# Kernel optimization log

Measured on AMD Instinct MI355X. Metric: run time of the kernel, lower is better.

Reference implementation:

```python
import jax, jax.numpy as jnp
import numpy as np

HIDDEN = 512
N_DRUG = 2000
N_REACTION = 10000
N_EDGES = 400000


def setup_inputs() -> dict:
    key = jax.random.key(0)
    ks = jax.random.split(key, 6)
    z_drug = jax.random.normal(ks[0], (N_DRUG, HIDDEN), dtype=jnp.float32)
    z_reaction = jax.random.normal(ks[1], (N_REACTION, HIDDEN), dtype=jnp.float32)
    row = jax.random.randint(ks[2], (N_EDGES,), 0, N_DRUG, dtype=jnp.int64)
    col = jax.random.randint(ks[3], (N_EDGES,), 0, N_REACTION, dtype=jnp.int64)
    # Linear weights in torch layout: (out_features, in_features)
    W1 = jax.random.normal(ks[4], (HIDDEN, 2 * HIDDEN), dtype=jnp.float32) * (1.0 / np.sqrt(2 * HIDDEN))
    b1 = jnp.zeros((HIDDEN,), dtype=jnp.float32)
    W2 = jax.random.normal(ks[5], (1, HIDDEN), dtype=jnp.float32) * (1.0 / np.sqrt(HIDDEN))
    b2 = jnp.zeros((1,), dtype=jnp.float32)
    return {"z_drug": z_drug, "z_reaction": z_reaction, "row": row, "col": col,
            "W1": W1, "b1": b1, "W2": W2, "b2": b2}


def reference(z_drug, z_reaction, row, col, W1, b1, W2, b2):
    # gather + concat: [E, 2H]
    z = jnp.concatenate([z_drug[row], z_reaction[col]], axis=-1)
    h = jax.nn.relu(jnp.einsum('eh,oh->eo', z, W1) + b1)  # [E, H]
    out = jnp.einsum('eh,oh->eo', h, W2) + b2             # [E, 1]
    return out.reshape(-1)
```

## Files before the change

kernel.cpp:

```cpp
#include <hip/hip_runtime.h>
#include <stdint.h>

#define HIDDEN 512
#define NDRUG 2000
#define NREACT 10000
#define NEDGE 400000

#define NBKT 320
#define SLOT 2048
#define CSTRIDE 16
#define NSCAT 128
#define EPB ((NEDGE + NSCAT - 1) / NSCAT)

#define BPB2 2
#define EBLK (NBKT * BPB2)
#define MAXSL 1024
#define HRSTRIDE 520
#define ETHREADS 512

typedef __attribute__((ext_vector_type(8))) _Float16 f16x8;
typedef __attribute__((ext_vector_type(2))) _Float16 f16x2;
typedef __attribute__((ext_vector_type(4))) float f32x4;
typedef __attribute__((ext_vector_type(8))) float f32x8;
typedef __attribute__((ext_vector_type(4))) float float4v;
typedef __attribute__((ext_vector_type(4))) _Float16 f16x4;

#if defined(__has_builtin)
#if __has_builtin(__builtin_amdgcn_fdot2)
#define HAVE_FDOT2 1
#endif
#endif

__global__ __launch_bounds__(256) void w1prep(const float* __restrict__ W1,
                                              _Float16* __restrict__ WL,
                                              _Float16* __restrict__ WR,
                                              int* __restrict__ cursor) {
  const int b = blockIdx.x;
  const int tid = threadIdx.x;
  if (b < 128) {
    const int nth = 128 * 256;
    const int NQ = HIDDEN * 2 * HIDDEN / 4;
    for (int i = b * 256 + tid; i < NQ; i += nth) {
      int e = i * 4;
      int o = e >> 10, j = e & 1023;
      float4v v = *reinterpret_cast<const float4v*>(W1 + e);
      f16x4 q; q[0]=(_Float16)v[0]; q[1]=(_Float16)v[1]; q[2]=(_Float16)v[2]; q[3]=(_Float16)v[3];
      if (j < HIDDEN) *reinterpret_cast<f16x4*>(WL + o * HIDDEN + j) = q;
      else            *reinterpret_cast<f16x4*>(WR + o * HIDDEN + (j - HIDDEN)) = q;
    }
  } else {
    int i = (b - 128) * 256 + tid;
    if (i < NBKT) cursor[i * CSTRIDE] = i * SLOT;
  }
}

#define BM 64
#define BN 128
#define BK 32
#define GEMMBLKS 756

__global__ __launch_bounds__(256) void gemm_scatter(
    const float* __restrict__ z_drug, const float* __restrict__ z_react,
    const _Float16* __restrict__ BL, const _Float16* __restrict__ BR,
    const float* __restrict__ bias,
    const int* __restrict__ row, const int* __restrict__ col,
    _Float16* __restrict__ Hd, _Float16* __restrict__ Hr,
    int* __restrict__ cursor, uint64_t* __restrict__ pk)
{
  __shared__ _Float16 As[BM * BK];
  __shared__ _Float16 Bs[BN * BK];
  __shared__ int lhist[NBKT];
  __shared__ int lbase[NBKT];

  const int bid = blockIdx.x;
  const int tid = threadIdx.x;

  if (bid >= GEMMBLKS) {
    const int sb = bid - GEMMBLKS;
    const int e0 = sb * EPB;
    const int e1 = (e0 + EPB < NEDGE) ? e0 + EPB : NEDGE;
    for (int i = tid; i < NBKT; i += 256) lhist[i] = 0;
    __syncthreads();
    for (int e = e0 + tid; e < e1; e += 256)
      atomicAdd(&lhist[col[e] >> 5], 1);
    __syncthreads();
    for (int i = tid; i < NBKT; i += 256) {
      int cnt = lhist[i];
      lbase[i] = cnt ? atomicAdd(&cursor[i * CSTRIDE], cnt) : 0;
      lhist[i] = 0;
    }
    __syncthreads();
    for (int e = e0 + tid; e < e1; e += 256) {
      int c = col[e];
      int r = row[e];
      int bkt = c >> 5;
      int lo = atomicAdd(&lhist[bkt], 1);
      pk[lbase[bkt] + lo] = ((uint64_t)e << 25) | ((uint64_t)r << 14) | (uint64_t)c;
    }
    return;
  }

  const int z = (bid >= 128) ? 1 : 0;
  const int t = z ? bid - 128 : bid;
  const int mb = t >> 2;
  const int nb = t & 3;
  const int M = (z == 0) ? NDRUG : NREACT;
  const float* A = (z == 0) ? z_drug : z_react;
  const _Float16* B = (z == 0) ? BL : BR;
  _Float16* C = (z == 0) ? Hd : Hr;
  const bool has_bias = (z == 0);
  const int K = HIDDEN, N = HIDDEN;

  const int lane = tid & 63;
  const int wid = tid >> 6;
  const int wn = wid;

  f32x4 acc[4][2];
#pragma unroll
  for (int i = 0; i < 4; ++i)
#pragma unroll
    for (int j = 0; j < 2; ++j) acc[i][j] = (f32x4){0.f, 0.f, 0.f, 0.f};

  const int row0 = mb * BM;
  const int col0 = nb * BN;
  const int r0 = tid >> 2;
  const int q0 = tid & 3;
  const int srow = lane >> 2;
  const int scol = (lane & 3) * 8;

  for (int kt = 0; kt < K; kt += BK) {
    int rA = row0 + r0;
    rA = rA < M ? rA : M - 1;
    f32x8 va = *reinterpret_cast<const f32x8*>(A + (size_t)rA * K + kt + q0 * 8);
    f16x8 afh = __builtin_convertvector(va, f16x8);
    __syncthreads();
    *reinterpret_cast<f16x8*>(As + r0 * BK + q0 * 8) = afh;
#pragma unroll
    for (int i = 0; i < 2; ++i) {
      int rB = col0 + wid * 32 + i * 16 + srow;
      const _Float16* gB = B + (size_t)rB * K + kt + scol;
      _Float16* lB = Bs + (wid * 32 + i * 16) * BK;
      __builtin_amdgcn_global_load_lds(
          (const __attribute__((address_space(1))) void*)gB,
          (__attribute__((address_space(3))) void*)lB, 16, 0, 0);
    }
    __syncthreads();

    const int fr = lane & 15;
    const int kg = (lane >> 4) * 8;
    f16x8 af[4], bfr[2];
#pragma unroll
    for (int mi = 0; mi < 4; ++mi)
      af[mi] = *reinterpret_cast<const f16x8*>(As + (mi * 16 + fr) * BK + kg);
#pragma unroll
    for (int ni = 0; ni < 2; ++ni)
      bfr[ni] = *reinterpret_cast<const f16x8*>(Bs + (wn * 32 + ni * 16 + fr) * BK + kg);
#pragma unroll
    for (int mi = 0; mi < 4; ++mi)
#pragma unroll
      for (int ni = 0; ni < 2; ++ni)
        acc[mi][ni] = __builtin_amdgcn_mfma_f32_16x16x32_f16(af[mi], bfr[ni], acc[mi][ni], 0, 0, 0);
  }

  const int crow = (lane >> 4) * 4;
  const int ccol = lane & 15;
#pragma unroll
  for (int ni = 0; ni < 2; ++ni) {
    const int gc = col0 + wn * 32 + ni * 16 + ccol;
    const float bv = has_bias ? bias[gc] : 0.0f;
#pragma unroll
    for (int mi = 0; mi < 4; ++mi) {
#pragma unroll
      for (int j = 0; j < 4; ++j) {
        const int gr = row0 + mi * 16 + crow + j;
        if (gr < M) C[(size_t)gr * N + gc] = (_Float16)(acc[mi][ni][j] + bv);
      }
    }
  }
}

__global__ __launch_bounds__(ETHREADS) void edge_kernel(
    const _Float16* __restrict__ Hd, const _Float16* __restrict__ Hr,
    const uint64_t* __restrict__ pk, const int* __restrict__ cursor,
    const float* __restrict__ W2, const float* __restrict__ b2,
    float* __restrict__ out)
{
  __shared__ _Float16 hrs[32 * HRSTRIDE];
  __shared__ uint64_t raw[MAXSL];
  __shared__ uint64_t spk[MAXSL];
  __shared__ int qdesc[MAXSL / 4 + 32];
  __shared__ int cnt[32], cb[32], cnt2[32], qoff[32];
  __shared__ int nqs;

  const int bid = blockIdx.x;
  const int xcd = bid & 7;
  const int idx = bid >> 3;
  const int bucket = xcd * 40 + (idx >> 1);
  const int slice = idx & 1;
  const int base = bucket * SLOT;
  const int count = cursor[bucket * CSTRIDE] - base;
  const int per = (count + BPB2 - 1) / BPB2;
  const int s = slice * per;
  const int e_end0 = (s + per < count) ? s + per : count;
  const int n = (e_end0 > s) ? e_end0 - s : 0;

  const int tid = threadIdx.x;
  const int lane = tid & 63;
  const int li = lane & 15;
  const int wv = tid >> 6;
  const int gid = wv * 4 + (lane >> 4);

#pragma unroll
  for (int rr2 = 0; rr2 < 4; ++rr2) {
    int rr = wv * 4 + rr2;
    int gr = bucket * 32 + rr;
    gr = (gr < NREACT) ? gr : NREACT - 1;
    const _Float16* src = Hr + (size_t)gr * HIDDEN + lane * 8;
    _Float16* dst = hrs + rr * HRSTRIDE;
    __builtin_amdgcn_global_load_lds(
        (const __attribute__((address_space(1))) void*)src,
        (__attribute__((address_space(3))) void*)dst, 16, 0, 0);
  }

  f16x8 w2v[4];
#pragma unroll
  for (int k = 0; k < 4; ++k) {
    const float* p = W2 + li * 8 + k * 128;
    f16x8 q;
#pragma unroll
    for (int j = 0; j < 8; ++j) q[j] = (_Float16)p[j];
    w2v[k] = q;
  }
  const float bias2 = *b2;
  const f16x8 zero8 = (f16x8)(_Float16)0;

  if (tid < 32) { cnt[tid] = 0; cnt2[tid] = 0; }
  __syncthreads();
  for (int i = tid; i < n; i += ETHREADS) {
    uint64_t p = pk[base + s + i];
    raw[i] = p;
    atomicAdd(&cnt[(int)(p & 31)], 1);
  }
  __syncthreads();
  if (tid == 0) {
    int acc = 0, qa = 0;
    for (int j = 0; j < 32; ++j) {
      cb[j] = acc; acc += cnt[j];
      qoff[j] = qa; qa += (cnt[j] + 3) >> 2;
    }
    nqs = qa;
  }
  __syncthreads();
  for (int i = tid; i < n; i += ETHREADS) {
    uint64_t p = raw[i];
    int lc = (int)(p & 31);
    int lo = atomicAdd(&cnt2[lc], 1);
    spk[cb[lc] + lo] = p;
  }
  __syncthreads();
  if (tid < 32) {
    int j = tid, st = cb[j], len = cnt[j], o = qoff[j];
    for (int q = 0; q < len; q += 4) {
      int cn = len - q; cn = (cn < 4) ? cn : 4;
      qdesc[o++] = j | ((st + q) << 5) | (cn << 16);
    }
  }
  __syncthreads();

  const int nq = nqs;
  for (int q = gid; q < nq; q += 32) {
    const int d = qdesc[q];
    const int lc = d & 31;
    const int st = (d >> 5) & 2047;
    const int cn = (d >> 16) & 7;

    const _Float16* hd[4];
    int si[4];
#pragma unroll
    for (int j = 0; j < 4; ++j) {
      int jj = (j < cn) ? j : cn - 1;
      uint64_t p = spk[st + jj];
      si[j] = (int)(p >> 25);
      hd[j] = Hd + (size_t)((p >> 14) & 0x7FF) * HIDDEN;
    }

    f16x8 vd[4][4];
#pragma unroll
    for (int j = 0; j < 4; ++j)
#pragma unroll
      for (int k = 0; k < 4; ++k)
        vd[j][k] = *reinterpret_cast<const f16x8*>(hd[j] + li * 8 + k * 128);

    f16x8 hv[4];
#pragma unroll
    for (int k = 0; k < 4; ++k)
      hv[k] = *reinterpret_cast<const f16x8*>(hrs + lc * HRSTRIDE + li * 8 + k * 128);

    float acc[4] = {0.f, 0.f, 0.f, 0.f};
#pragma unroll
    for (int j = 0; j < 4; ++j) {
#pragma unroll
      for (int k = 0; k < 4; ++k) {
        f16x8 t = __builtin_elementwise_max(vd[j][k] + hv[k], zero8);
#if defined(HAVE_FDOT2)
#pragma unroll
        for (int qq = 0; qq < 4; ++qq) {
          f16x2 wp = {w2v[k][2 * qq], w2v[k][2 * qq + 1]};
          f16x2 sp = {t[2 * qq], t[2 * qq + 1]};
          acc[j] = __builtin_amdgcn_fdot2(sp, wp, acc[j], false);
        }
#else
#pragma unroll
        for (int qq = 0; qq < 8; ++qq)
          acc[j] += (float)t[qq] * (float)w2v[k][qq];
#endif
      }
    }
#pragma unroll
    for (int off = 8; off >= 1; off >>= 1) {
#pragma unroll
      for (int j = 0; j < 4; ++j) acc[j] += __shfl_xor(acc[j], off);
    }
    if (li == 0) {
      for (int j = 0; j < cn; ++j) out[si[j]] = acc[j] + bias2;
    }
  }
}

extern "C" void kernel_launch(void* const* d_in, const int* in_sizes, int n_in,
                              void* d_out, int out_size, void* d_ws, size_t ws_size,
                              hipStream_t stream) {
  const float* z_drug  = (const float*)d_in[0];
  const float* z_react = (const float*)d_in[1];
  const int*   row     = (const int*)d_in[2];
  const int*   col     = (const int*)d_in[3];
  const float* W1      = (const float*)d_in[4];
  const float* b1      = (const float*)d_in[5];
  const float* W2      = (const float*)d_in[6];
  const float* b2      = (const float*)d_in[7];
  float* out = (float*)d_out;

  char* ws = (char*)d_ws;
  size_t off = 0;
  auto alloc = [&](size_t bytes) {
    void* p = ws + off;
    off += (bytes + 255) & ~(size_t)255;
    return p;
  };
  _Float16* wl_f = (_Float16*)alloc((size_t)HIDDEN * HIDDEN * 2);
  _Float16* wr_f = (_Float16*)alloc((size_t)HIDDEN * HIDDEN * 2);
  _Float16* Hd   = (_Float16*)alloc((size_t)NDRUG * HIDDEN * 2);
  _Float16* Hr   = (_Float16*)alloc((size_t)NREACT * HIDDEN * 2);
  int*      cursor = (int*)alloc((size_t)NBKT * CSTRIDE * 4);
  uint64_t* pk     = (uint64_t*)alloc((size_t)NBKT * SLOT * 8);

  w1prep<<<130, 256, 0, stream>>>(W1, wl_f, wr_f, cursor);
  gemm_scatter<<<GEMMBLKS + NSCAT, 256, 0, stream>>>(z_drug, z_react, wl_f, wr_f, b1,
                                                     row, col, Hd, Hr, cursor, pk);
  edge_kernel<<<EBLK, ETHREADS, 0, stream>>>(Hd, Hr, pk, cursor, W2, b2, out);
}
```

Before: 67.41 us.

## Use 40-column reaction buckets and keep packed edges in registers

Regroups reaction columns into 250 buckets of 40 rows each (via a multiply-shift divide by 40) instead of 320 buckets of 32, so each edge block stages 40 Hr rows in LDS and the grid remaps buckets across XCDs to match. The edge kernel also holds up to two packed edges per thread in registers instead of a shared raw[] staging array, which drops one LDS round trip and frees shared memory. The cost is a larger per-block load and more edges per bucket. Correctness depends on the slice count staying at or below 1024, since each thread now handles only two edges.

```diff
diff --git a/kernel.cpp b/kernel.cpp
--- a/kernel.cpp
+++ b/kernel.cpp
@@ -6,7 +6,8 @@
 #define NREACT 10000
 #define NEDGE 400000
 
-#define NBKT 320
+#define NBKT 250
+#define HRROWS 40
 #define SLOT 2048
 #define CSTRIDE 16
 #define NSCAT 128
@@ -17,6 +18,8 @@
 #define MAXSL 1024
 #define HRSTRIDE 520
 #define ETHREADS 512
+
+__device__ __forceinline__ int col2bkt(int c) { return (c * 6554) >> 18; }
 
 typedef __attribute__((ext_vector_type(8))) _Float16 f16x8;
 typedef __attribute__((ext_vector_type(2))) _Float16 f16x2;
@@ -69,8 +72,8 @@
 {
   __shared__ _Float16 As[BM * BK];
   __shared__ _Float16 Bs[BN * BK];
-  __shared__ int lhist[NBKT];
-  __shared__ int lbase[NBKT];
+  __shared__ int lhist[256];
+  __shared__ int lbase[256];
 
   const int bid = blockIdx.x;
   const int tid = threadIdx.x;
@@ -79,21 +82,21 @@
     const int sb = bid - GEMMBLKS;
     const int e0 = sb * EPB;
     const int e1 = (e0 + EPB < NEDGE) ? e0 + EPB : NEDGE;
-    for (int i = tid; i < NBKT; i += 256) lhist[i] = 0;
+    if (tid < 256) { lhist[tid] = 0; }
     __syncthreads();
     for (int e = e0 + tid; e < e1; e += 256)
-      atomicAdd(&lhist[col[e] >> 5], 1);
-    __syncthreads();
-    for (int i = tid; i < NBKT; i += 256) {
-      int cnt = lhist[i];
-      lbase[i] = cnt ? atomicAdd(&cursor[i * CSTRIDE], cnt) : 0;
-      lhist[i] = 0;
+      atomicAdd(&lhist[col2bkt(col[e])], 1);
+    __syncthreads();
+    if (tid < NBKT) {
+      int cnt = lhist[tid];
+      lbase[tid] = cnt ? atomicAdd(&cursor[tid * CSTRIDE], cnt) : 0;
+      lhist[tid] = 0;
     }
     __syncthreads();
     for (int e = e0 + tid; e < e1; e += 256) {
       int c = col[e];
       int r = row[e];
-      int bkt = c >> 5;
+      int bkt = col2bkt(c);
       int lo = atomicAdd(&lhist[bkt], 1);
       pk[lbase[bkt] + lo] = ((uint64_t)e << 25) | ((uint64_t)r << 14) | (uint64_t)c;
     }
@@ -185,18 +188,19 @@
     const float* __restrict__ W2, const float* __restrict__ b2,
     float* __restrict__ out)
 {
-  __shared__ _Float16 hrs[32 * HRSTRIDE];
-  __shared__ uint64_t raw[MAXSL];
+  __shared__ _Float16 hrs[HRROWS * HRSTRIDE];
   __shared__ uint64_t spk[MAXSL];
-  __shared__ int qdesc[MAXSL / 4 + 32];
-  __shared__ int cnt[32], cb[32], cnt2[32], qoff[32];
+  __shared__ int qdesc[MAXSL / 4 + HRROWS];
+  __shared__ int cnt[HRROWS], cb[HRROWS], cnt2[HRROWS], qoff[HRROWS];
   __shared__ int nqs;
 
   const int bid = blockIdx.x;
-  const int xcd = bid & 7;
-  const int idx = bid >> 3;
-  const int bucket = xcd * 40 + (idx >> 1);
-  const int slice = idx & 1;
+  const int porig = bid >> 1;
+  const int slice = bid & 1;
+  const int xcd = porig & 7;
+  const int pidx = porig >> 3;
+  const int bucket = (xcd < 2 ? xcd * 32 : 2 * 32 + (xcd - 2) * 31) + pidx;
+  const int cbase = bucket * HRROWS;
   const int base = bucket * SLOT;
   const int count = cursor[bucket * CSTRIDE] - base;
   const int per = (count + BPB2 - 1) / BPB2;
@@ -211,10 +215,9 @@
   const int gid = wv * 4 + (lane >> 4);
 
 #pragma unroll
-  for (int rr2 = 0; rr2 < 4; ++rr2) {
-    int rr = wv * 4 + rr2;
-    int gr = bucket * 32 + rr;
-    gr = (gr < NREACT) ? gr : NREACT - 1;
+  for (int rr2 = 0; rr2 < 5; ++rr2) {
+    int rr = wv * 5 + rr2;
+    int gr = cbase + rr;
     const _Float16* src = Hr + (size_t)gr * HIDDEN + lane * 8;
     _Float16* dst = hrs + rr * HRSTRIDE;
     __builtin_amdgcn_global_load_lds(
@@ -234,35 +237,39 @@
   const float bias2 = *b2;
   const f16x8 zero8 = (f16x8)(_Float16)0;
 
-  if (tid < 32) { cnt[tid] = 0; cnt2[tid] = 0; }
-  __syncthreads();
-  for (int i = tid; i < n; i += ETHREADS) {
-    uint64_t p = pk[base + s + i];
-    raw[i] = p;
-    atomicAdd(&cnt[(int)(p & 31)], 1);
+  if (tid < HRROWS) { cnt[tid] = 0; cnt2[tid] = 0; }
+  __syncthreads();
+  uint64_t p0 = 0, p1 = 0;
+  int b0 = 0, b1 = 0;
+  const int i0 = tid, i1 = tid + ETHREADS;
+  if (i0 < n) {
+    p0 = pk[base + s + i0];
+    b0 = (int)(p0 & 0x3FFF) - cbase;
+    atomicAdd(&cnt[b0], 1);
+  }
+  if (i1 < n) {
+    p1 = pk[base + s + i1];
+    b1 = (int)(p1 & 0x3FFF) - cbase;
+    atomicAdd(&cnt[b1], 1);
   }
   __syncthreads();
   if (tid == 0) {
     int acc = 0, qa = 0;
-    for (int j = 0; j < 32; ++j) {
+    for (int j = 0; j < HRROWS; ++j) {
       cb[j] = acc; acc += cnt[j];
       qoff[j] = qa; qa += (cnt[j] + 3) >> 2;
     }
     nqs = qa;
   }
   __syncthreads();
-  for (int i = tid; i < n; i += ETHREADS) {
-    uint64_t p = raw[i];
-    int lc = (int)(p & 31);
-    int lo = atomicAdd(&cnt2[lc], 1);
-    spk[cb[lc] + lo] = p;
-  }
-  __syncthreads();
-  if (tid < 32) {
+  if (i0 < n) { int lo = atomicAdd(&cnt2[b0], 1); spk[cb[b0] + lo] = p0; }
+  if (i1 < n) { int lo = atomicAdd(&cnt2[b1], 1); spk[cb[b1] + lo] = p1; }
+  __syncthreads();
+  if (tid < HRROWS) {
     int j = tid, st = cb[j], len = cnt[j], o = qoff[j];
     for (int q = 0; q < len; q += 4) {
       int cn = len - q; cn = (cn < 4) ? cn : 4;
-      qdesc[o++] = j | ((st + q) << 5) | (cn << 16);
+      qdesc[o++] = j | ((st + q) << 6) | (cn << 17);
     }
   }
   __syncthreads();
@@ -270,9 +277,9 @@
   const int nq = nqs;
   for (int q = gid; q < nq; q += 32) {
     const int d = qdesc[q];
-    const int lc = d & 31;
-    const int st = (d >> 5) & 2047;
-    const int cn = (d >> 16) & 7;
+    const int lc = d & 63;
+    const int st = (d >> 6) & 2047;
+    const int cn = (d >> 17) & 7;
 
     const _Float16* hd[4];
     int si[4];
```

Result: faster. 62.88 us (-6.7%).
